# Optimization experiments

Hardware: AMD Instinct MI355X
Metric: run time of the kernel (lower is better)

Reference implementation:

```python
import jax, jax.numpy as jnp
import numpy as np

EPS = 1e-5
HALT_THRESHOLD = 0.01
DILATIONS = (1, 2, 4)


def layer_norm(x, g, b):
    m = jnp.mean(x, axis=-1, keepdims=True)
    v = jnp.var(x, axis=-1, keepdims=True)
    return (x - m) * jax.lax.rsqrt(v + EPS) * g + b


def depthwise_conv(x, k, dilation):
    # x: [B,H,W,C], k: [kh,kw,1,C] (groups == C)
    pad = dilation * (k.shape[0] // 2)
    return jax.lax.conv_general_dilated(
        x, k, window_strides=(1, 1), padding=[(pad, pad), (pad, pad)],
        rhs_dilation=(dilation, dilation),
        dimension_numbers=('NHWC', 'HWIO', 'NHWC'),
        feature_group_count=x.shape[-1])


def setup_inputs() -> dict:
    key = jax.random.key(0)
    ks = jax.random.split(key, 12)
    B, H, W, C = 8, 96, 96, 64
    hid = 64
    P = C + len(DILATIONS) * C  # 256
    n = jax.random.normal
    return {
        'x': n(ks[0], (B, H, W, C), dtype=jnp.float32),
        'g1': jnp.ones((C,), jnp.float32), 'b1': jnp.zeros((C,), jnp.float32),
        'g2': jnp.ones((P,), jnp.float32), 'b2': jnp.zeros((P,), jnp.float32),
        'k1': 0.2 * n(ks[1], (3, 3, 1, C), dtype=jnp.float32),
        'k2': 0.2 * n(ks[2], (3, 3, 1, C), dtype=jnp.float32),
        'k3': 0.2 * n(ks[3], (3, 3, 1, C), dtype=jnp.float32),
        'Wu1': n(ks[4], (P, 2 * hid), dtype=jnp.float32) / np.sqrt(P),
        'bu1': jnp.zeros((2 * hid,), jnp.float32),
        'Wu2': n(ks[5], (2 * hid, hid), dtype=jnp.float32) / np.sqrt(2 * hid),
        'bu2': jnp.zeros((hid,), jnp.float32),
        'Wu3': n(ks[6], (hid, C), dtype=jnp.float32) / np.sqrt(hid),
        'bu3': jnp.zeros((C,), jnp.float32),
        'gh': jnp.ones((C,), jnp.float32), 'bh': jnp.zeros((C,), jnp.float32),
        'Wh1': n(ks[7], (C, hid), dtype=jnp.float32) / np.sqrt(C),
        'bh1': jnp.zeros((hid,), jnp.float32),
        'Wh2': n(ks[8], (hid, 1), dtype=jnp.float32) / np.sqrt(hid),
        'bh2': jnp.zeros((1,), jnp.float32),
        'max_steps': 8, 'min_steps': 1,
    }


def reference(x, g1, b1, g2, b2, k1, k2, k3, Wu1, bu1, Wu2, bu2, Wu3, bu3,
              gh, bh, Wh1, bh1, Wh2, bh2, max_steps, min_steps):
    gelu = lambda t: jax.nn.gelu(t, approximate=False)

    def forward_step(xs):
        # halt unit: LN -> Linear -> GELU -> Linear -> sigmoid
        h = gelu(layer_norm(xs, gh, bh) @ Wh1 + bh1)
        halt_probs = jax.nn.sigmoid(h @ Wh2 + bh2)[..., 0]  # [B,H,W]
        xn = layer_norm(xs, g1, b1)
        ps = [depthwise_conv(xn, k, d) for k, d in zip((k1, k2, k3), DILATIONS)]
        u = layer_norm(jnp.concatenate([xn] + ps, axis=-1), g2, b2)
        h1 = gelu(u @ Wu1 + bu1)
        h2 = gelu(h1 @ Wu2 + bu2)
        delta = h2 @ Wu3 + bu3
        return delta, halt_probs

    B, H, W, C = x.shape
    halted0 = jnp.zeros((B, H, W), jnp.bool_)
    acc0 = jnp.zeros((B, H, W), x.dtype)
    so0 = jnp.zeros_like(x)
    pc0 = jnp.zeros((B, H, W), x.dtype)

    def body(carry, step):
        xs, halted, acc, so, pc = carry
        delta, hp = forward_step(xs)
        active = ~halted
        af = active.astype(xs.dtype)
        xs = xs + delta * af[..., None]
        in_halt_phase = step >= (min_steps - 1)
        acc_n = acc + hp * af
        should_halt = (acc_n > 1.0 - HALT_THRESHOLD) & active
        halt_w = jnp.where(should_halt, 1.0 - (acc_n - hp), hp * af)
        so_n = so + xs * halt_w[..., None]
        halted_n = halted | should_halt
        acc = jnp.where(in_halt_phase, acc_n, acc)
        so = jnp.where(in_halt_phase, so_n, so)
        halted = jnp.where(in_halt_phase, halted_n, halted)
        pc = pc + jnp.where(in_halt_phase, af, jnp.ones_like(pc))
        return (xs, halted, acc, so, pc), None

    (xf, halted, acc, so, pc), _ = jax.lax.scan(
        body, (x, halted0, acc0, so0, pc0), jnp.arange(max_steps))
    # distribute remaining probability mass to cells that never halted
    remaining_w = (~halted).astype(x.dtype) * (1.0 - acc)
    so = so + xf * remaining_w[..., None]
    pc = pc / max_steps
    return so, halted, pc
```

## Files before the change

### kernel.cpp

```cpp
#include <hip/hip_runtime.h>
#include <hip/hip_bf16.h>

#define NPIX 73728
#define CH 64
#define HH 96
#define WW 96
#define PP 256

typedef __attribute__((ext_vector_type(8))) short short8;
typedef __attribute__((ext_vector_type(4))) float f32x4;

__device__ __forceinline__ float wsum64(float v) {
#pragma unroll
  for (int off = 32; off > 0; off >>= 1) v += __shfl_xor(v, off, 64);
  return v;
}
__device__ __forceinline__ float wsum16(float v) {
#pragma unroll
  for (int off = 1; off < 16; off <<= 1) v += __shfl_xor(v, off, 64);
  return v;
}
__device__ __forceinline__ float gelu_f(float x) {
  return 0.5f * x * (1.0f + erff(x * 0.70710678118654752f));
}
__device__ __forceinline__ float b2f(ushort u) {
  union { unsigned int i; float f; } c;
  c.i = ((unsigned int)u) << 16;
  return c.f;
}
__device__ __forceinline__ ushort f2b(float f) {
  union { float f; unsigned int i; } c;
  c.f = f;
  unsigned int r = c.i + 0x7fff + ((c.i >> 16) & 1);
  return (ushort)(r >> 16);
}

__global__ __launch_bounds__(256) void k_init(const float* __restrict__ x,
                                              float* __restrict__ xs,
                                              float* __restrict__ out,
                                              float* __restrict__ accb,
                                              float* __restrict__ xnf) {
  int i = blockIdx.x * 256 + threadIdx.x;
  if (i < NPIX * CH) xs[i] = x[i];
  if (i < NPIX * 66) out[i] = 0.0f;
  if (i < NPIX) { accb[i] = 0.0f; xnf[i] = 0.0f; }
}

__global__ __launch_bounds__(256) void k_wprep(const float* __restrict__ W,
                                               ushort* __restrict__ Wp, int K,
                                               int N) {
  int t = blockIdx.x * 256 + threadIdx.x;
  if (t >= K * N) return;
  int j = t & 7, l = (t >> 3) & 63, tile = t >> 9;
  int NT = N >> 4;
  int kt = tile / NT, nt = tile - kt * NT;
  int k = kt * 32 + ((l >> 4) & 3) * 8 + j;
  int n = nt * 16 + (l & 15);
  Wp[t] = f2b(W[k * N + n]);
}

__global__ __launch_bounds__(256) void k_ln_halt(
    const float* __restrict__ xs, ushort* __restrict__ xn, float* __restrict__ hp,
    const float* __restrict__ halted, float* __restrict__ xnf,
    const float* __restrict__ g1, const float* __restrict__ b1,
    const float* __restrict__ gh, const float* __restrict__ bh,
    const float* __restrict__ Wh1, const float* __restrict__ bh1,
    const float* __restrict__ Wh2, const float* __restrict__ bh2) {
  __shared__ float lnbuf[4][64];
  int wave = threadIdx.x >> 6, lane = threadIdx.x & 63;
  int pix = blockIdx.x * 4 + wave;
  float hf = halted[pix];
  if (hf != 0.0f && xnf[pix] != 0.0f) return;
  float x = xs[(size_t)pix * CH + lane];
  float mean = wsum64(x) * (1.0f / 64.0f);
  float d = x - mean;
  float var = wsum64(d * d) * (1.0f / 64.0f);
  float rstd = rsqrtf(var + 1e-5f);
  float nrm = d * rstd;
  xn[(size_t)pix * CH + lane] = f2b(nrm * g1[lane] + b1[lane]);
  lnbuf[wave][lane] = nrm * gh[lane] + bh[lane];
  float acc = bh1[lane];
#pragma unroll 8
  for (int i = 0; i < 64; ++i)
    acc = fmaf(lnbuf[wave][i], Wh1[i * 64 + lane], acc);
  acc = gelu_f(acc);
  float c = wsum64(acc * Wh2[lane]);
  if (lane == 0) {
    hp[pix] = 1.0f / (1.0f + expf(-(c + bh2[0])));
    xnf[pix] = hf;
  }
}

template <bool EDGE>
__device__ __forceinline__ void do_taps(const ushort* pb,
                                        const float* __restrict__ k1,
                                        const float* __restrict__ k2,
                                        const float* __restrict__ k3, int cg,
                                        int y, int xq, float (&br)[4][4]) {
#pragma unroll
  for (int t = 0; t < 3; ++t) {
    const int dl = (t == 0) ? 1 : ((t == 1) ? 2 : 4);
    const float* kk = (t == 0) ? k1 : ((t == 1) ? k2 : k3);
    float a0 = 0.f, a1 = 0.f, a2 = 0.f, a3 = 0.f;
#pragma unroll
    for (int ky = 0; ky < 3; ++ky) {
#pragma unroll
      for (int kx = 0; kx < 3; ++kx) {
        const int dy = (ky - 1) * dl, dx = (kx - 1) * dl;
        if (EDGE && !(ky == 1 && kx == 1)) {
          if ((unsigned)(y + dy) >= HH) continue;
        }
        const float4 w = *(const float4*)&kk[(ky * 3 + kx) * CH + cg * 4];
        float v0, v1, v2, v3;
        if (ky == 1 && kx == 1) {
          v0 = br[0][0]; v1 = br[0][1]; v2 = br[0][2]; v3 = br[0][3];
        } else {
          ushort4 d4 = *(const ushort4*)(pb + (dy * WW + dx) * CH);
          v0 = b2f(d4.x); v1 = b2f(d4.y); v2 = b2f(d4.z); v3 = b2f(d4.w);
          if (EDGE && (unsigned)(xq + dx) >= WW) {
            v0 = 0.f; v1 = 0.f; v2 = 0.f; v3 = 0.f;
          }
        }
        a0 = fmaf(v0, w.x, a0); a1 = fmaf(v1, w.y, a1);
        a2 = fmaf(v2, w.z, a2); a3 = fmaf(v3, w.w, a3);
      }
    }
    br[t + 1][0] = a0; br[t + 1][1] = a1;
    br[t + 1][2] = a2; br[t + 1][3] = a3;
  }
}

__global__ __launch_bounds__(256) void k_conv_u(
    const ushort* __restrict__ xn, ushort* __restrict__ u,
    const float* __restrict__ halted,
    const float* __restrict__ k1, const float* __restrict__ k2,
    const float* __restrict__ k3, const float* __restrict__ g2,
    const float* __restrict__ b2) {
  int wv = threadIdx.x >> 6, l = threadIdx.x & 63;
  int pix0 = blockIdx.x * 16 + wv * 4;
  int px = l >> 4, cg = l & 15;
  int pix = pix0 + px;
  float hfp = halted[pix];
  if (__all(hfp != 0.0f)) return;
  if (hfp != 0.0f) return;
  int b = pix0 / (HH * WW);
  int rem = pix0 - b * (HH * WW);
  int y = rem / WW, x0 = rem - (rem / WW) * WW;
  int xq = x0 + px;
  const ushort* pb = xn + (size_t)pix * CH + cg * 4;

  float br[4][4];
  {
    ushort4 c4 = *(const ushort4*)pb;
    br[0][0] = b2f(c4.x); br[0][1] = b2f(c4.y);
    br[0][2] = b2f(c4.z); br[0][3] = b2f(c4.w);
  }
  bool interior = (x0 >= 4) && (x0 <= WW - 8) && (y >= 4) && (y <= HH - 5);
  if (interior)
    do_taps<false>(pb, k1, k2, k3, cg, y, xq, br);
  else
    do_taps<true>(pb, k1, k2, k3, cg, y, xq, br);

  float s = 0.f;
#pragma unroll
  for (int t = 0; t < 4; ++t)
#pragma unroll
    for (int c = 0; c < 4; ++c) s += br[t][c];
  float mean = wsum16(s) * (1.0f / 256.0f);
  float vs = 0.f;
#pragma unroll
  for (int t = 0; t < 4; ++t)
#pragma unroll
    for (int c = 0; c < 4; ++c) {
      float d = br[t][c] - mean;
      vs += d * d;
    }
  float rstd = rsqrtf(wsum16(vs) * (1.0f / 256.0f) + 1e-5f);
  ushort* ub = u + (size_t)blockIdx.x * 4096;
  int lr16 = pix & 15;
#pragma unroll
  for (int t = 0; t < 4; ++t) {
    float4 g = *(const float4*)&g2[t * CH + cg * 4];
    float4 bb = *(const float4*)&b2[t * CH + cg * 4];
    ushort4 o;
    o.x = f2b((br[t][0] - mean) * rstd * g.x + bb.x);
    o.y = f2b((br[t][1] - mean) * rstd * g.y + bb.y);
    o.z = f2b((br[t][2] - mean) * rstd * g.z + bb.z);
    o.w = f2b((br[t][3] - mean) * rstd * g.w + bb.w);
    int k0 = t * 64 + cg * 4;
    int kt = k0 >> 5, lg = (k0 >> 3) & 3, jj = k0 & 7;
    *(ushort4*)(ub + kt * 512 + (lg * 16 + lr16) * 8 + jj) = o;
  }
}

__global__ __launch_bounds__(64) void k_mlp(
    const ushort* __restrict__ u, const ushort* __restrict__ Wp1,
    const ushort* __restrict__ Wp2, const ushort* __restrict__ Wp3,
    const float* __restrict__ bu1, const float* __restrict__ bu2,
    const float* __restrict__ bu3, const float* __restrict__ hp,
    float* __restrict__ xs, float* __restrict__ so, float* __restrict__ halted,
    float* __restrict__ accb, float* __restrict__ pc,
    const int* __restrict__ min_steps, int step) {
  __shared__ ushort h1s[16 * 136];
  __shared__ ushort h2s[16 * 72];
  int l = threadIdx.x;
  int p0 = blockIdx.x * 16;
  int lr = l & 15, lg = l >> 4;
  if (__all(halted[p0 + lr] != 0.0f)) return;
  const f32x4 vzero = {0.0f, 0.0f, 0.0f, 0.0f};

  const ushort* ub = u + (size_t)blockIdx.x * 4096 + l * 8;
  short8 a[8];
#pragma unroll
  for (int kt = 0; kt < 8; ++kt) a[kt] = *(const short8*)(ub + kt * 512);
  f32x4 acc1[8];
#pragma unroll
  for (int nt = 0; nt < 8; ++nt) acc1[nt] = vzero;
#pragma unroll
  for (int kt = 0; kt < 8; ++kt) {
#pragma unroll
    for (int nt = 0; nt < 8; ++nt) {
      short8 b = *(const short8*)(Wp1 + ((kt * 8 + nt) * 64 + l) * 8);
      acc1[nt] = __builtin_amdgcn_mfma_f32_16x16x32_bf16(a[kt], b, acc1[nt], 0, 0, 0);
    }
  }
  ushort* h1w = h1s;
#pragma unroll
  for (int nt = 0; nt < 8; ++nt) {
    float bb = bu1[nt * 16 + lr];
#pragma unroll
    for (int i = 0; i < 4; ++i)
      h1w[(lg * 4 + i) * 136 + nt * 16 + lr] = f2b(gelu_f(acc1[nt][i] + bb));
  }

  f32x4 acc2[4];
#pragma unroll
  for (int nt = 0; nt < 4; ++nt) acc2[nt] = vzero;
#pragma unroll
  for (int kt = 0; kt < 4; ++kt) {
    short8 av = *(const short8*)(h1w + lr * 136 + kt * 32 + lg * 8);
#pragma unroll
    for (int nt = 0; nt < 4; ++nt) {
      short8 b = *(const short8*)(Wp2 + ((kt * 4 + nt) * 64 + l) * 8);
      acc2[nt] = __builtin_amdgcn_mfma_f32_16x16x32_bf16(av, b, acc2[nt], 0, 0, 0);
    }
  }
  ushort* h2w = h2s;
#pragma unroll
  for (int nt = 0; nt < 4; ++nt) {
    float bb = bu2[nt * 16 + lr];
#pragma unroll
    for (int i = 0; i < 4; ++i)
      h2w[(lg * 4 + i) * 72 + nt * 16 + lr] = f2b(gelu_f(acc2[nt][i] + bb));
  }

  f32x4 acc3[4];
#pragma unroll
  for (int nt = 0; nt < 4; ++nt) acc3[nt] = vzero;
#pragma unroll
  for (int kt = 0; kt < 2; ++kt) {
    short8 av = *(const short8*)(h2w + lr * 72 + kt * 32 + lg * 8);
#pragma unroll
    for (int nt = 0; nt < 4; ++nt) {
      short8 b = *(const short8*)(Wp3 + ((kt * 4 + nt) * 64 + l) * 8);
      acc3[nt] = __builtin_amdgcn_mfma_f32_16x16x32_bf16(av, b, acc3[nt], 0, 0, 0);
    }
  }
  float* df = (float*)h1w;
#pragma unroll
  for (int nt = 0; nt < 4; ++nt) {
    float bb = bu3[nt * 16 + lr];
#pragma unroll
    for (int i = 0; i < 4; ++i)
      df[(lg * 4 + i) * 68 + nt * 16 + lr] = acc3[nt][i] + bb;
  }

  int msteps = min_steps[0];
  bool in_halt = (step >= msteps - 1);
  int px = l >> 2, q = l & 3;
  int p = p0 + px;
  float hf = halted[p];
  if (hf == 0.0f) {
    float hpv = hp[p];
    float accv = accb[p];
    float acc_n = accv + hpv;
    bool should_halt = (acc_n > 0.99f);
    float halt_w = should_halt ? (1.0f - (acc_n - hpv)) : hpv;
    size_t base = (size_t)p * CH + q * 16;
#pragma unroll
    for (int j = 0; j < 4; ++j) {
      float4 dv = *(const float4*)&df[px * 68 + q * 16 + j * 4];
      float4 xv = *(float4*)&xs[base + j * 4];
      xv.x += dv.x;
      xv.y += dv.y;
      xv.z += dv.z;
      xv.w += dv.w;
      *(float4*)&xs[base + j * 4] = xv;
      if (in_halt) {
        float4 sv = *(float4*)&so[base + j * 4];
        sv.x += xv.x * halt_w;
        sv.y += xv.y * halt_w;
        sv.z += xv.z * halt_w;
        sv.w += xv.w * halt_w;
        *(float4*)&so[base + j * 4] = sv;
      }
    }
    if (q == 0) {
      if (in_halt) {
        accb[p] = acc_n;
        halted[p] = should_halt ? 1.0f : 0.0f;
      }
      pc[p] += 1.0f;
    }
  } else if (q == 0 && !in_halt) {
    pc[p] += 1.0f;
  }
}

__global__ __launch_bounds__(256) void k_final(
    const float* __restrict__ xs, float* __restrict__ so,
    const float* __restrict__ halted, const float* __restrict__ accb,
    float* __restrict__ pc, const int* __restrict__ max_steps) {
  int wave = threadIdx.x >> 6, lane = threadIdx.x & 63;
  int pix = blockIdx.x * 4 + wave;
  float rem = (halted[pix] == 0.0f) ? (1.0f - accb[pix]) : 0.0f;
  so[(size_t)pix * CH + lane] += xs[(size_t)pix * CH + lane] * rem;
  if (lane == 0) pc[pix] *= 1.0f / (float)max_steps[0];
}

extern "C" void kernel_launch(void* const* d_in, const int* in_sizes, int n_in,
                              void* d_out, int out_size, void* d_ws,
                              size_t ws_size, hipStream_t stream) {
  const float* x   = (const float*)d_in[0];
  const float* g1  = (const float*)d_in[1];
  const float* b1  = (const float*)d_in[2];
  const float* g2  = (const float*)d_in[3];
  const float* b2  = (const float*)d_in[4];
  const float* k1  = (const float*)d_in[5];
  const float* k2  = (const float*)d_in[6];
  const float* k3  = (const float*)d_in[7];
  const float* Wu1 = (const float*)d_in[8];
  const float* bu1 = (const float*)d_in[9];
  const float* Wu2 = (const float*)d_in[10];
  const float* bu2 = (const float*)d_in[11];
  const float* Wu3 = (const float*)d_in[12];
  const float* bu3 = (const float*)d_in[13];
  const float* gh  = (const float*)d_in[14];
  const float* bh  = (const float*)d_in[15];
  const float* Wh1 = (const float*)d_in[16];
  const float* bh1 = (const float*)d_in[17];
  const float* Wh2 = (const float*)d_in[18];
  const float* bh2 = (const float*)d_in[19];
  const int* max_steps = (const int*)d_in[20];
  const int* min_steps = (const int*)d_in[21];

  if (ws_size < (size_t)68000000) return;
  char* ws = (char*)d_ws;
  float*  xs   = (float*)(ws);
  ushort* xn   = (ushort*)(ws + 18874368);
  ushort* u    = (ushort*)(ws + 28311552);
  float*  hp   = (float*)(ws + 66060288);
  float*  accb = (float*)(ws + 66355200);
  ushort* Wp1  = (ushort*)(ws + 66650112);
  ushort* Wp2  = (ushort*)(ws + 66715648);
  ushort* Wp3  = (ushort*)(ws + 66732032);
  float*  xnf  = (float*)(ws + 66740224);
  float* so = (float*)d_out;
  float* halted = so + (size_t)NPIX * CH;
  float* pc = halted + NPIX;

  k_wprep<<<128, 256, 0, stream>>>(Wu1, Wp1, 256, 128);
  k_wprep<<<32, 256, 0, stream>>>(Wu2, Wp2, 128, 64);
  k_wprep<<<16, 256, 0, stream>>>(Wu3, Wp3, 64, 64);
  k_init<<<19008, 256, 0, stream>>>(x, xs, so, accb, xnf);
  for (int step = 0; step < 8; ++step) {
    k_ln_halt<<<NPIX / 4, 256, 0, stream>>>(xs, xn, hp, halted, xnf, g1, b1,
                                            gh, bh, Wh1, bh1, Wh2, bh2);
    k_conv_u<<<NPIX / 16, 256, 0, stream>>>(xn, u, halted, k1, k2, k3, g2, b2);
    k_mlp<<<NPIX / 16, 64, 0, stream>>>(u, Wp1, Wp2, Wp3, bu1, bu2, bu3, hp,
                                        xs, so, halted, accb, pc, min_steps,
                                        step);
  }
  k_final<<<NPIX / 4, 256, 0, stream>>>(xs, so, halted, accb, pc, max_steps);
}
```

Before: 694.3 us.

## Compact active pixels into an index list for the conv and MLP stages

```diff
diff --git a/kernel.cpp b/kernel.cpp
--- a/kernel.cpp
+++ b/kernel.cpp
@@ -39,11 +39,13 @@
                                               float* __restrict__ xs,
                                               float* __restrict__ out,
                                               float* __restrict__ accb,
-                                              float* __restrict__ xnf) {
+                                              float* __restrict__ xnf,
+                                              int* __restrict__ cnt) {
   int i = blockIdx.x * 256 + threadIdx.x;
   if (i < NPIX * CH) xs[i] = x[i];
   if (i < NPIX * 66) out[i] = 0.0f;
   if (i < NPIX) { accb[i] = 0.0f; xnf[i] = 0.0f; }
+  if (i < 8) cnt[i] = 0;
 }
 
 __global__ __launch_bounds__(256) void k_wprep(const float* __restrict__ W,
@@ -57,6 +59,23 @@
   int k = kt * 32 + ((l >> 4) & 3) * 8 + j;
   int n = nt * 16 + (l & 15);
   Wp[t] = f2b(W[k * N + n]);
+}
+
+__global__ __launch_bounds__(256) void k_compact(const float* __restrict__ halted,
+                                                 int* __restrict__ cnt,
+                                                 int* __restrict__ idx, int step) {
+  int p = blockIdx.x * 256 + threadIdx.x;
+  bool active = (halted[p] == 0.0f);
+  unsigned long long mask = __ballot(active);
+  int lane = threadIdx.x & 63;
+  int cw = __popcll(mask);
+  int wbase = 0;
+  if (lane == 0 && cw) wbase = atomicAdd(&cnt[step], cw);
+  wbase = __shfl(wbase, 0, 64);
+  if (active) {
+    int off = __popcll(mask & ((1ull << lane) - 1ull));
+    idx[wbase + off] = p;
+  }
 }
 
 __global__ __launch_bounds__(256) void k_ln_halt(
@@ -132,21 +151,20 @@
 
 __global__ __launch_bounds__(256) void k_conv_u(
     const ushort* __restrict__ xn, ushort* __restrict__ u,
-    const float* __restrict__ halted,
+    const int* __restrict__ idx, const int* __restrict__ cnt, int step,
     const float* __restrict__ k1, const float* __restrict__ k2,
     const float* __restrict__ k3, const float* __restrict__ g2,
     const float* __restrict__ b2) {
+  int n = cnt[step];
+  if (blockIdx.x * 16 >= n) return;
   int wv = threadIdx.x >> 6, l = threadIdx.x & 63;
-  int pix0 = blockIdx.x * 16 + wv * 4;
-  int px = l >> 4, cg = l & 15;
-  int pix = pix0 + px;
-  float hfp = halted[pix];
-  if (__all(hfp != 0.0f)) return;
-  if (hfp != 0.0f) return;
-  int b = pix0 / (HH * WW);
-  int rem = pix0 - b * (HH * WW);
-  int y = rem / WW, x0 = rem - (rem / WW) * WW;
-  int xq = x0 + px;
+  int cpx = l >> 4, cg = l & 15;
+  int slot = blockIdx.x * 16 + wv * 4 + cpx;
+  bool live = slot < n;
+  int pix = idx[live ? slot : (n - 1)];
+  int b = pix / (HH * WW);
+  int rem = pix - b * (HH * WW);
+  int y = rem / WW, xq = rem - (rem / WW) * WW;
   const ushort* pb = xn + (size_t)pix * CH + cg * 4;
 
   float br[4][4];
@@ -155,8 +173,8 @@
     br[0][0] = b2f(c4.x); br[0][1] = b2f(c4.y);
     br[0][2] = b2f(c4.z); br[0][3] = b2f(c4.w);
   }
-  bool interior = (x0 >= 4) && (x0 <= WW - 8) && (y >= 4) && (y <= HH - 5);
-  if (interior)
+  bool interior = (xq >= 4) && (xq <= WW - 5) && (y >= 4) && (y <= HH - 5);
+  if (__all(interior))
     do_taps<false>(pb, k1, k2, k3, cg, y, xq, br);
   else
     do_taps<true>(pb, k1, k2, k3, cg, y, xq, br);
@@ -177,36 +195,39 @@
     }
   float rstd = rsqrtf(wsum16(vs) * (1.0f / 256.0f) + 1e-5f);
   ushort* ub = u + (size_t)blockIdx.x * 4096;
-  int lr16 = pix & 15;
-#pragma unroll
-  for (int t = 0; t < 4; ++t) {
-    float4 g = *(const float4*)&g2[t * CH + cg * 4];
-    float4 bb = *(const float4*)&b2[t * CH + cg * 4];
-    ushort4 o;
-    o.x = f2b((br[t][0] - mean) * rstd * g.x + bb.x);
-    o.y = f2b((br[t][1] - mean) * rstd * g.y + bb.y);
-    o.z = f2b((br[t][2] - mean) * rstd * g.z + bb.z);
-    o.w = f2b((br[t][3] - mean) * rstd * g.w + bb.w);
-    int k0 = t * 64 + cg * 4;
-    int kt = k0 >> 5, lg = (k0 >> 3) & 3, jj = k0 & 7;
-    *(ushort4*)(ub + kt * 512 + (lg * 16 + lr16) * 8 + jj) = o;
+  int lr16 = wv * 4 + cpx;
+  if (live) {
+#pragma unroll
+    for (int t = 0; t < 4; ++t) {
+      float4 g = *(const float4*)&g2[t * CH + cg * 4];
+      float4 bb = *(const float4*)&b2[t * CH + cg * 4];
+      ushort4 o;
+      o.x = f2b((br[t][0] - mean) * rstd * g.x + bb.x);
+      o.y = f2b((br[t][1] - mean) * rstd * g.y + bb.y);
+      o.z = f2b((br[t][2] - mean) * rstd * g.z + bb.z);
+      o.w = f2b((br[t][3] - mean) * rstd * g.w + bb.w);
+      int k0 = t * 64 + cg * 4;
+      int kt = k0 >> 5, lg = (k0 >> 3) & 3, jj = k0 & 7;
+      *(ushort4*)(ub + kt * 512 + (lg * 16 + lr16) * 8 + jj) = o;
+    }
   }
 }
 
 __global__ __launch_bounds__(64) void k_mlp(
-    const ushort* __restrict__ u, const ushort* __restrict__ Wp1,
+    const ushort* __restrict__ u, const int* __restrict__ idx,
+    const int* __restrict__ cnt, int step, const ushort* __restrict__ Wp1,
     const ushort* __restrict__ Wp2, const ushort* __restrict__ Wp3,
     const float* __restrict__ bu1, const float* __restrict__ bu2,
     const float* __restrict__ bu3, const float* __restrict__ hp,
     float* __restrict__ xs, float* __restrict__ so, float* __restrict__ halted,
     float* __restrict__ accb, float* __restrict__ pc,
-    const int* __restrict__ min_steps, int step) {
+    const int* __restrict__ min_steps) {
+  int n = cnt[step];
+  if (blockIdx.x * 16 >= n) return;
   __shared__ ushort h1s[16 * 136];
   __shared__ ushort h2s[16 * 72];
   int l = threadIdx.x;
-  int p0 = blockIdx.x * 16;
   int lr = l & 15, lg = l >> 4;
-  if (__all(halted[p0 + lr] != 0.0f)) return;
   const f32x4 vzero = {0.0f, 0.0f, 0.0f, 0.0f};
 
   const ushort* ub = u + (size_t)blockIdx.x * 4096 + l * 8;
@@ -278,9 +299,9 @@
   int msteps = min_steps[0];
   bool in_halt = (step >= msteps - 1);
   int px = l >> 2, q = l & 3;
-  int p = p0 + px;
-  float hf = halted[p];
-  if (hf == 0.0f) {
+  int slot = blockIdx.x * 16 + px;
+  if (slot < n) {
+    int p = idx[slot];
     float hpv = hp[p];
     float accv = accb[p];
     float acc_n = accv + hpv;
@@ -312,8 +333,6 @@
       }
       pc[p] += 1.0f;
     }
-  } else if (q == 0 && !in_halt) {
-    pc[p] += 1.0f;
   }
 }
 
@@ -365,6 +384,8 @@
   ushort* Wp2  = (ushort*)(ws + 66715648);
   ushort* Wp3  = (ushort*)(ws + 66732032);
   float*  xnf  = (float*)(ws + 66740224);
+  int*    idx  = (int*)(ws + 67035136);
+  int*    cnt  = (int*)(ws + 67330048);
   float* so = (float*)d_out;
   float* halted = so + (size_t)NPIX * CH;
   float* pc = halted + NPIX;
@@ -372,14 +393,16 @@
   k_wprep<<<128, 256, 0, stream>>>(Wu1, Wp1, 256, 128);
   k_wprep<<<32, 256, 0, stream>>>(Wu2, Wp2, 128, 64);
   k_wprep<<<16, 256, 0, stream>>>(Wu3, Wp3, 64, 64);
-  k_init<<<19008, 256, 0, stream>>>(x, xs, so, accb, xnf);
+  k_init<<<19008, 256, 0, stream>>>(x, xs, so, accb, xnf, cnt);
   for (int step = 0; step < 8; ++step) {
+    k_compact<<<NPIX / 256, 256, 0, stream>>>(halted, cnt, idx, step);
     k_ln_halt<<<NPIX / 4, 256, 0, stream>>>(xs, xn, hp, halted, xnf, g1, b1,
                                             gh, bh, Wh1, bh1, Wh2, bh2);
-    k_conv_u<<<NPIX / 16, 256, 0, stream>>>(xn, u, halted, k1, k2, k3, g2, b2);
-    k_mlp<<<NPIX / 16, 64, 0, stream>>>(u, Wp1, Wp2, Wp3, bu1, bu2, bu3, hp,
-                                        xs, so, halted, accb, pc, min_steps,
-                                        step);
+    k_conv_u<<<NPIX / 16, 256, 0, stream>>>(xn, u, idx, cnt, step, k1, k2, k3,
+                                            g2, b2);
+    k_mlp<<<NPIX / 16, 64, 0, stream>>>(u, idx, cnt, step, Wp1, Wp2, Wp3, bu1,
+                                        bu2, bu3, hp, xs, so, halted, accb, pc,
+                                        min_steps);
   }
   k_final<<<NPIX / 4, 256, 0, stream>>>(xs, so, halted, accb, pc, max_steps);
 }
```

After: 710.7 us. 2.4% more time.
